# Optimization experiments

Hardware: AMD Instinct MI355X
Metric: run time of the kernel (lower is better)

## Reference

```python
import jax, jax.numpy as jnp
import numpy as np

B, T, E, S = 16, 2048, 1024, 2000
HID = 150
GI = 3 * E


def _mlp(x, W1, b1, W2, b2, W3, b3):
    # Score module: Linear->ReLU->(Dropout eval=id)->Linear->ReLU->(Dropout)->Linear(->1)
    h = jax.nn.relu(x @ W1 + b1)
    h = jax.nn.relu(h @ W2 + b2)
    return h @ W3 + b3


def setup_inputs() -> dict:
    key = jax.random.key(0)
    ks = jax.random.split(key, 16)
    batch_embeds = jax.random.normal(ks[0], (B, T, E), dtype=jnp.float32)
    starts = jnp.sort(jax.random.randint(ks[1], (B, S), 0, T - 33), axis=-1)
    lengths = jax.random.randint(ks[2], (B, S), 0, 24)
    num_spans = jax.random.randint(ks[3], (B,), 1, S + 1)
    sc = 0.02
    p = lambda k, shape: jax.random.normal(k, shape, dtype=jnp.float32) * sc
    return {
        "batch_embeds": batch_embeds,
        "starts": starts,
        "lengths": lengths,
        "num_spans": num_spans,
        "Wa1": p(ks[4], (E, HID)), "ba1": jnp.zeros((HID,), jnp.float32),
        "Wa2": p(ks[5], (HID, HID)), "ba2": jnp.zeros((HID,), jnp.float32),
        "Wa3": p(ks[6], (HID, 1)), "ba3": jnp.zeros((1,), jnp.float32),
        "Ws1": p(ks[7], (GI, HID)), "bs1": jnp.zeros((HID,), jnp.float32),
        "Ws2": p(ks[8], (HID, HID)), "bs2": jnp.zeros((HID,), jnp.float32),
        "Ws3": p(ks[9], (HID, 1)), "bs3": jnp.zeros((1,), jnp.float32),
    }


def reference(batch_embeds, starts, lengths, num_spans,
              Wa1, ba1, Wa2, ba2, Wa3, ba3,
              Ws1, bs1, Ws2, bs2, Ws3, bs3):
    # attention score per token: [B,T,1]
    attns = _mlp(batch_embeds, Wa1, ba1, Wa2, ba2, Wa3, ba3)
    weighted = batch_embeds * attns  # [B,T,E]
    # prefix sums turn the ragged per-span sum into two gathers per span
    csum = jnp.cumsum(weighted, axis=1)
    csum = jnp.concatenate([jnp.zeros_like(csum[:, :1]), csum], axis=1)  # [B,T+1,E]
    ends = starts + lengths  # inclusive end index, < T
    g_start = jnp.take_along_axis(batch_embeds, starts[..., None], axis=1)  # [B,S,E]
    g_end = jnp.take_along_axis(batch_embeds, ends[..., None], axis=1)      # [B,S,E]
    span_sum = (jnp.take_along_axis(csum, (ends + 1)[..., None], axis=1)
                - jnp.take_along_axis(csum, starts[..., None], axis=1))     # [B,S,E]
    span_emb = jnp.concatenate([g_start, g_end, span_sum], axis=-1)  # [B,S,3E]
    # zero-pad spans beyond each document's span count (matches torch zeros padding)
    mask = (jnp.arange(span_emb.shape[1])[None, :] < num_spans[:, None])[..., None]
    span_emb = jnp.where(mask, span_emb, jnp.zeros((), span_emb.dtype))
    mention_scores = _mlp(span_emb, Ws1, bs1, Ws2, bs2, Ws3, bs3)  # [B,S,1]
    return span_emb, mention_scores
```

## Files before the change

kernel.cpp:

```cpp
#include <hip/hip_runtime.h>
#include <hip/hip_bf16.h>

#define B_   16
#define T_   2048
#define E_   1024
#define S_   2000
#define HID_ 150
#define GI_  3072

typedef __attribute__((ext_vector_type(8))) short short8;
typedef __attribute__((ext_vector_type(4))) float f32x4;

constexpr int NPAD  = 160;
constexpr int LSTR  = 168;
constexpr int MROWS = 64;

__device__ __forceinline__ void gload16(const void* gsrc, void* ldst) {
    __builtin_amdgcn_global_load_lds(
        (const __attribute__((address_space(1))) unsigned int*)gsrc,
        (__attribute__((address_space(3))) unsigned int*)ldst,
        16, 0, 0);
}

__device__ __forceinline__ short8 pack8(float4 a, float4 b) {
    union { __hip_bfloat162 h[4]; short8 s; } u;
    u.h[0] = __float22bfloat162_rn(make_float2(a.x, a.y));
    u.h[1] = __float22bfloat162_rn(make_float2(a.z, a.w));
    u.h[2] = __float22bfloat162_rn(make_float2(b.x, b.y));
    u.h[3] = __float22bfloat162_rn(make_float2(b.z, b.w));
    return u.s;
}

__device__ __forceinline__ short8 pack8v(f32x4 a, f32x4 b) {
    union { __hip_bfloat162 h[4]; short8 s; } u;
    u.h[0] = __float22bfloat162_rn(make_float2(a.x, a.y));
    u.h[1] = __float22bfloat162_rn(make_float2(a.z, a.w));
    u.h[2] = __float22bfloat162_rn(make_float2(b.x, b.y));
    u.h[3] = __float22bfloat162_rn(make_float2(b.z, b.w));
    return u.s;
}

__device__ __forceinline__ void bf16x8_f32(short8 m, f32x4& lo, f32x4& hi) {
    union { short8 s; __hip_bfloat162 h[4]; } u; u.s = m;
    float2 f0 = __bfloat1622float2(u.h[0]);
    float2 f1 = __bfloat1622float2(u.h[1]);
    float2 f2 = __bfloat1622float2(u.h[2]);
    float2 f3 = __bfloat1622float2(u.h[3]);
    lo = (f32x4){f0.x, f0.y, f1.x, f1.y};
    hi = (f32x4){f2.x, f2.y, f3.x, f3.y};
}

__global__ __launch_bounds__(256)
void transpose_all(const float* __restrict__ Wa1, const float* __restrict__ Wa2,
                   const float* __restrict__ Ws1, const float* __restrict__ Ws2,
                   __hip_bfloat16* __restrict__ Wt1a, __hip_bfloat16* __restrict__ Wt2a,
                   __hip_bfloat16* __restrict__ Wt1s, __hip_bfloat16* __restrict__ Wt2s,
                   float* __restrict__ zerobuf)
{
    const int s0 = 160 * 1024, s1 = 160 * 160, s2 = 160 * 3072, s3 = 160 * 160;
    int i = blockIdx.x * 256 + threadIdx.x;
    if (i < s0) {
        int n = i >> 10, k = i & 1023;
        Wt1a[i] = __float2bfloat16(n < HID_ ? Wa1[k * HID_ + n] : 0.f);
    } else if (i < s0 + s1) {
        int j = i - s0, n = j / 160, k = j - n * 160;
        Wt2a[j] = __float2bfloat16((n < HID_ && k < HID_) ? Wa2[k * HID_ + n] : 0.f);
    } else if (i < s0 + s1 + s2) {
        int j = i - s0 - s1, n = j / 3072, k = j - n * 3072;
        Wt1s[j] = __float2bfloat16(n < HID_ ? Ws1[k * HID_ + n] : 0.f);
    } else if (i < s0 + s1 + s2 + s3) {
        int j = i - s0 - s1 - s2, n = j / 160, k = j - n * 160;
        Wt2s[j] = __float2bfloat16((n < HID_ && k < HID_) ? Ws2[k * HID_ + n] : 0.f);
    } else if (i < s0 + s1 + s2 + s3 + 1024) {
        zerobuf[i - s0 - s1 - s2 - s3] = 0.f;
    }
}

template<int K1>
__global__ __launch_bounds__(256, 2)
void mlp_mfma(const float* __restrict__ xin,
              const __hip_bfloat16* __restrict__ Wt1, const float* __restrict__ b1,
              const __hip_bfloat16* __restrict__ Wt2, const float* __restrict__ b2,
              const float* __restrict__ W3, const float* __restrict__ b3,
              float* __restrict__ outp)
{
    constexpr int NC  = K1 / 64;
    constexpr int ACH = 64 * 64 * 4;
    constexpr int BCH = 160 * 64 * 2;
    __shared__ __align__(16) char smem[2 * ACH + 2 * BCH];

    const int tid  = threadIdx.x;
    const int lane = tid & 63;
    const int w    = tid >> 6;
    const int rg   = w >> 1;
    const int cg   = w & 1;
    const int lr   = lane & 15;
    const int hi   = lane >> 4;

    const long long row0 = (long long)blockIdx.x * MROWS;

    auto stageA = [&](int bi, int c) {
        char* dst = smem + bi * ACH;
#pragma unroll
        for (int j = 0; j < 4; ++j) {
            const int row  = (w * 4 + j) * 4 + (lane >> 4);
            const int slot = (lane & 15) ^ (row & 7);
            gload16(xin + (row0 + row) * (long long)K1 + c * 64 + slot * 4,
                    dst + (w * 4 + j) * 1024);
        }
    };
    auto stageB = [&](int bi, int c) {
        char* dst = smem + 2 * ACH + bi * BCH;
#pragma unroll
        for (int j = 0; j < 5; ++j) {
            const int nrow = (w * 5 + j) * 8 + (lane >> 3);
            const int slot = (lane & 7) ^ (nrow & 7);
            gload16(Wt1 + (long long)nrow * K1 + c * 64 + slot * 8,
                    dst + (w * 5 + j) * 1024);
        }
    };

    f32x4 acc[2][5];
#pragma unroll
    for (int rt = 0; rt < 2; ++rt)
#pragma unroll
        for (int nt = 0; nt < 5; ++nt) acc[rt][nt] = (f32x4){0.f, 0.f, 0.f, 0.f};

    stageA(0, 0);
    stageB(0, 0);

    for (int c = 0; c < NC; ++c) {
        __syncthreads();
        if (c + 1 < NC) { stageA((c + 1) & 1, c + 1); stageB((c + 1) & 1, c + 1); }
        const int bi = c & 1;
        const char* sA = smem + bi * ACH;
        const char* sB = smem + 2 * ACH + bi * BCH;
#pragma unroll
        for (int ks = 0; ks < 2; ++ks) {
            short8 bfr[5];
#pragma unroll
            for (int nt = 0; nt < 5; ++nt) {
                const int nrow = cg * 80 + nt * 16 + lr;
                const int slot = (ks * 4 + hi) ^ (nrow & 7);
                bfr[nt] = *(const short8*)(sB + nrow * 128 + slot * 16);
            }
#pragma unroll
            for (int rt = 0; rt < 2; ++rt) {
                const int r = rg * 32 + rt * 16 + lr;
                const int s0i = (ks * 8 + hi * 2) ^ (r & 7);
                const int s1i = (ks * 8 + hi * 2 + 1) ^ (r & 7);
                float4 a0 = *(const float4*)(sA + r * 256 + s0i * 16);
                float4 a1 = *(const float4*)(sA + r * 256 + s1i * 16);
                short8 afr = pack8(a0, a1);
#pragma unroll
                for (int nt = 0; nt < 5; ++nt)
                    acc[rt][nt] = __builtin_amdgcn_mfma_f32_16x16x32_bf16(
                        afr, bfr[nt], acc[rt][nt], 0, 0, 0);
            }
        }
    }
    __syncthreads();

    __hip_bfloat16* hl = (__hip_bfloat16*)smem;

#pragma unroll
    for (int nt = 0; nt < 5; ++nt) {
        const int ch = cg * 80 + nt * 16 + lr;
        const float bb = (ch < HID_) ? b1[ch] : 0.f;
#pragma unroll
        for (int rt = 0; rt < 2; ++rt)
#pragma unroll
            for (int r4 = 0; r4 < 4; ++r4) {
                const int row = rg * 32 + rt * 16 + hi * 4 + r4;
                float h = acc[rt][nt][r4] + bb;
                hl[row * LSTR + ch] = __float2bfloat16(h > 0.f ? h : 0.f);
            }
    }
    __syncthreads();

    f32x4 acc2[2][5];
#pragma unroll
    for (int rt = 0; rt < 2; ++rt)
#pragma unroll
        for (int nt = 0; nt < 5; ++nt) acc2[rt][nt] = (f32x4){0.f, 0.f, 0.f, 0.f};

#pragma unroll
    for (int ks = 0; ks < 5; ++ks) {
        const int k0 = ks * 32 + hi * 8;
        short8 bfr[5];
#pragma unroll
        for (int nt = 0; nt < 5; ++nt)
            bfr[nt] = *(const short8*)(Wt2 + (cg * 80 + nt * 16 + lr) * NPAD + k0);
#pragma unroll
        for (int rt = 0; rt < 2; ++rt) {
            short8 afr = *(const short8*)&hl[(rg * 32 + rt * 16 + lr) * LSTR + k0];
#pragma unroll
            for (int nt = 0; nt < 5; ++nt)
                acc2[rt][nt] = __builtin_amdgcn_mfma_f32_16x16x32_bf16(
                    afr, bfr[nt], acc2[rt][nt], 0, 0, 0);
        }
    }
    __syncthreads();

#pragma unroll
    for (int nt = 0; nt < 5; ++nt) {
        const int ch = cg * 80 + nt * 16 + lr;
        const float bb = (ch < HID_) ? b2[ch] : 0.f;
#pragma unroll
        for (int rt = 0; rt < 2; ++rt)
#pragma unroll
            for (int r4 = 0; r4 < 4; ++r4) {
                const int row = rg * 32 + rt * 16 + hi * 4 + r4;
                float h = acc2[rt][nt][r4] + bb;
                hl[row * LSTR + ch] = __float2bfloat16(h > 0.f ? h : 0.f);
            }
    }
    __syncthreads();

    {
        const int row = tid >> 2, quad = tid & 3;
        const int kb = quad * 38;
        const int ke = (kb + 38 > HID_) ? HID_ : kb + 38;
        float s = 0.f;
        for (int k = kb; k < ke; ++k)
            s += __bfloat162float(hl[row * LSTR + k]) * W3[k];
        s += __shfl_xor(s, 1);
        s += __shfl_xor(s, 2);
        if (quad == 0) outp[row0 + row] = s + b3[0];
    }
}

__global__ __launch_bounds__(256)
void wsum_tiles(const float* __restrict__ x, const float* __restrict__ attn,
                float* __restrict__ P)
{
    const int b = blockIdx.x >> 5, tile = blockIdx.x & 31, q = threadIdx.x;
    const float* xb = x + ((long long)b * T_ + tile * 64) * E_ + q * 4;
    const float* ab = attn + b * T_ + tile * 64;
    f32x4 a0 = (f32x4){0.f, 0.f, 0.f, 0.f}, a1 = a0;
#pragma unroll 8
    for (int t = 0; t < 64; t += 2) {
        a0 += ab[t]     * *(const f32x4*)(xb + (long long)t * E_);
        a1 += ab[t + 1] * *(const f32x4*)(xb + (long long)(t + 1) * E_);
    }
    *(f32x4*)(P + ((long long)(b * 32 + tile)) * E_ + q * 4) = a0 + a1;
}

__global__ __launch_bounds__(256)
void wcumsum(const float* __restrict__ x, const float* __restrict__ attn,
             const float* __restrict__ P, __hip_bfloat16* __restrict__ csum)
{
    const int b = blockIdx.x >> 5, tile = blockIdx.x & 31, q = threadIdx.x;
    f32x4 pfx = (f32x4){0.f, 0.f, 0.f, 0.f};
    for (int tau = 0; tau < tile; ++tau)
        pfx += *(const f32x4*)(P + ((long long)(b * 32 + tau)) * E_ + q * 4);
    const float* xb = x + ((long long)b * T_ + tile * 64) * E_ + q * 4;
    __hip_bfloat16* cb = csum + ((long long)b * T_ + tile * 64) * E_ + q * 4;
    const float* ab = attn + b * T_ + tile * 64;
    f32x4 acc = pfx;
#pragma unroll 4
    for (int t = 0; t < 64; ++t) {
        acc += ab[t] * *(const f32x4*)(xb + (long long)t * E_);
        union { __hip_bfloat162 h[2]; uint2 u; } cv;
        cv.h[0] = __float22bfloat162_rn(make_float2(acc.x, acc.y));
        cv.h[1] = __float22bfloat162_rn(make_float2(acc.z, acc.w));
        *(uint2*)(cb + (long long)t * E_) = cv.u;
    }
}

__global__ __launch_bounds__(512, 4)
void span_score(const float* __restrict__ x, const __hip_bfloat16* __restrict__ csum,
                const float* __restrict__ zrow,
                const int* __restrict__ starts, const int* __restrict__ lengths,
                const int* __restrict__ nspans,
                const __hip_bfloat16* __restrict__ Wt1, const float* __restrict__ b1,
                const __hip_bfloat16* __restrict__ Wt2, const float* __restrict__ b2,
                const float* __restrict__ W3, const float* __restrict__ b3,
                float* __restrict__ spanout, float* __restrict__ scoreout)
{
    __shared__ __align__(16) char smem[58112];
    int* stL = (int*)(smem + 57344);
    int* enL = (int*)(smem + 57600);
    int* bL  = (int*)(smem + 57856);

    const int tid  = threadIdx.x;
    const int lane = tid & 63;
    const int w    = tid >> 6;
    const int rg   = w >> 1;
    const int cg   = w & 1;
    const int lr   = lane & 15;
    const int hi   = lane >> 4;

    int bid = blockIdx.x;
    {
        const int qq = 500 / 8, rr = 500 % 8;
        const int xcd = bid % 8, i = bid / 8;
        bid = (xcd < rr ? xcd * (qq + 1) : rr * (qq + 1) + (xcd - rr) * qq) + i;
    }
    const int span0 = bid * 64;

    if (tid < 64) {
        const int sp = span0 + tid;
        const int b  = sp / S_;
        const int s  = sp - b * S_;
        const bool val = s < nspans[b];
        const int st = val ? starts[sp] : 0;
        stL[tid] = st;
        enL[tid] = val ? (st + lengths[sp]) : -1;
        bL[tid]  = b;
    }
    __syncthreads();

    const int r    = tid >> 3;
    const int q    = tid & 7;
    const int st_r = stL[r];
    const int en_r = enL[r];
    const bool valid = en_r >= st_r;
    const long long sp_r = span0 + r;
    const float* xb = x + (long long)bL[r] * T_ * E_;
    const __hip_bfloat16* cbh = csum + (long long)bL[r] * T_ * E_;
    const __hip_bfloat16* zrh = (const __hip_bfloat16*)zrow;

    const float* px_st = valid ? xb + (long long)st_r * E_ : zrow;
    const float* px_en = valid ? xb + (long long)en_r * E_ : zrow;
    const __hip_bfloat16* pc_en = valid ? cbh + (long long)en_r * E_ : zrh;
    const __hip_bfloat16* pc_st = (valid && st_r > 0) ? cbh + (long long)(st_r - 1) * E_ : zrh;

    auto ldreg = [&](int c, f32x4& l0, f32x4& l1, short8& m0, short8& m1) {
        const int off = (c & 15) * 64 + q * 8;
        if (c < 32) {
            const float* s1 = (c < 16) ? px_st : px_en;
            l0 = *(const f32x4*)(s1 + off);
            l1 = *(const f32x4*)(s1 + off + 4);
        } else {
            m0 = *(const short8*)(pc_en + off);
            m1 = *(const short8*)(pc_st + off);
        }
    };
    auto emit = [&](int bi, int c, f32x4 l0, f32x4 l1, short8 m0, short8 m1) {
        f32x4 v0, v1;
        if (c < 32) { v0 = l0; v1 = l1; }
        else {
            f32x4 e0, e1, s0, s1v;
            bf16x8_f32(m0, e0, e1);
            bf16x8_f32(m1, s0, s1v);
            v0 = e0 - s0; v1 = e1 - s1v;
        }
        float* orow = spanout + sp_r * (3 * E_) + c * 64 + q * 8;
        *(f32x4*)orow       = v0;
        *(f32x4*)(orow + 4) = v1;
        *(short8*)(smem + bi * 8192 + r * 128 + ((q ^ (r & 7)) * 16)) = pack8v(v0, v1);
    };
    auto stageB = [&](int bi, int c) {
        char* dst = smem + 16384 + bi * 20480;
#pragma unroll
        for (int j = 0; j < 3; ++j) {
            const int idx = w * 3 + j;
            if (idx < 20) {
                const int nrow = idx * 8 + (lane >> 3);
                const int slot = (lane & 7) ^ (nrow & 7);
                gload16(Wt1 + (long long)nrow * GI_ + c * 64 + slot * 8,
                        dst + idx * 1024);
            }
        }
    };

    f32x4 acc[5];
#pragma unroll
    for (int nt = 0; nt < 5; ++nt) acc[nt] = (f32x4){0.f, 0.f, 0.f, 0.f};

    f32x4 pA0, pA1;  short8 mA0, mA1;
    f32x4 pB0, pB1;  short8 mB0, mB1;

    stageB(0, 0);
    asm volatile("" ::: "memory");
    ldreg(0, pA0, pA1, mA0, mA1);
    emit(0, 0, pA0, pA1, mA0, mA1);
    ldreg(1, pB0, pB1, mB0, mB1);

    auto mfma_block = [&](int bi) {
        const char* sAc = smem + bi * 8192;
        const char* sBc = smem + 16384 + bi * 20480;
#pragma unroll
        for (int ks = 0; ks < 2; ++ks) {
            short8 bfr[5];
#pragma unroll
            for (int nt = 0; nt < 5; ++nt) {
                const int nrow = cg * 80 + nt * 16 + lr;
                const int slot = (ks * 4 + hi) ^ (nrow & 7);
                bfr[nt] = *(const short8*)(sBc + nrow * 128 + slot * 16);
            }
            const int r2 = rg * 16 + lr;
            const int sl = (ks * 4 + hi) ^ (r2 & 7);
            short8 afr = *(const short8*)(sAc + r2 * 128 + sl * 16);
#pragma unroll
            for (int nt = 0; nt < 5; ++nt)
                acc[nt] = __builtin_amdgcn_mfma_f32_16x16x32_bf16(
                    afr, bfr[nt], acc[nt], 0, 0, 0);
        }
    };

    auto phase = [&](int c, f32x4& u0, f32x4& u1, short8& um0, short8& um1,
                     f32x4& f0, f32x4& f1, short8& fm0, short8& fm1) {
        asm volatile("s_waitcnt vmcnt(4) lgkmcnt(0)" ::: "memory");
        __builtin_amdgcn_s_barrier();
        const int bi = c & 1;
        if (c + 1 < 48) {
            stageB(bi ^ 1, c + 1);
            asm volatile("" ::: "memory");
            if (c + 2 < 48) ldreg(c + 2, f0, f1, fm0, fm1);
            asm volatile("" ::: "memory");
            emit(bi ^ 1, c + 1, u0, u1, um0, um1);
        }
        mfma_block(bi);
    };

    for (int cc = 0; cc < 46; cc += 2) {
        phase(cc,     pB0, pB1, mB0, mB1, pA0, pA1, mA0, mA1);
        phase(cc + 1, pA0, pA1, mA0, mA1, pB0, pB1, mB0, mB1);
    }
    phase(46, pB0, pB1, mB0, mB1, pA0, pA1, mA0, mA1);
    asm volatile("s_waitcnt vmcnt(2) lgkmcnt(0)" ::: "memory");
    __builtin_amdgcn_s_barrier();
    mfma_block(1);

    asm volatile("s_waitcnt lgkmcnt(0)" ::: "memory");
    __builtin_amdgcn_s_barrier();

    __hip_bfloat16* hl = (__hip_bfloat16*)smem;

#pragma unroll
    for (int nt = 0; nt < 5; ++nt) {
        const int ch = cg * 80 + nt * 16 + lr;
        const float bb = (ch < HID_) ? b1[ch] : 0.f;
#pragma unroll
        for (int r4 = 0; r4 < 4; ++r4) {
            const int row = rg * 16 + hi * 4 + r4;
            float h = acc[nt][r4] + bb;
            hl[row * LSTR + ch] = __float2bfloat16(h > 0.f ? h : 0.f);
        }
    }
    __syncthreads();

    f32x4 acc2[5];
#pragma unroll
    for (int nt = 0; nt < 5; ++nt) acc2[nt] = (f32x4){0.f, 0.f, 0.f, 0.f};

#pragma unroll
    for (int ks = 0; ks < 5; ++ks) {
        const int k0 = ks * 32 + hi * 8;
        short8 bfr[5];
#pragma unroll
        for (int nt = 0; nt < 5; ++nt)
            bfr[nt] = *(const short8*)(Wt2 + (cg * 80 + nt * 16 + lr) * NPAD + k0);
        short8 afr = *(const short8*)&hl[(rg * 16 + lr) * LSTR + k0];
#pragma unroll
        for (int nt = 0; nt < 5; ++nt)
            acc2[nt] = __builtin_amdgcn_mfma_f32_16x16x32_bf16(
                afr, bfr[nt], acc2[nt], 0, 0, 0);
    }
    __syncthreads();

#pragma unroll
    for (int nt = 0; nt < 5; ++nt) {
        const int ch = cg * 80 + nt * 16 + lr;
        const float bb = (ch < HID_) ? b2[ch] : 0.f;
#pragma unroll
        for (int r4 = 0; r4 < 4; ++r4) {
            const int row = rg * 16 + hi * 4 + r4;
            float h = acc2[nt][r4] + bb;
            hl[row * LSTR + ch] = __float2bfloat16(h > 0.f ? h : 0.f);
        }
    }
    __syncthreads();

    {
        const int row = tid >> 3, oct = tid & 7;
        const int kb = oct * 19;
        const int ke = (kb + 19 > HID_) ? HID_ : kb + 19;
        float s = 0.f;
        for (int k = kb; k < ke; ++k)
            s += __bfloat162float(hl[row * LSTR + k]) * W3[k];
        s += __shfl_xor(s, 1);
        s += __shfl_xor(s, 2);
        s += __shfl_xor(s, 4);
        if (oct == 0) scoreout[span0 + row] = s + b3[0];
    }
}

extern "C" void kernel_launch(void* const* d_in, const int* in_sizes, int n_in,
                              void* d_out, int out_size, void* d_ws, size_t ws_size,
                              hipStream_t stream) {
    const float* x       = (const float*)d_in[0];
    const int*   starts  = (const int*)d_in[1];
    const int*   lengths = (const int*)d_in[2];
    const int*   nspans  = (const int*)d_in[3];
    const float* Wa1 = (const float*)d_in[4];
    const float* ba1 = (const float*)d_in[5];
    const float* Wa2 = (const float*)d_in[6];
    const float* ba2 = (const float*)d_in[7];
    const float* Wa3 = (const float*)d_in[8];
    const float* ba3 = (const float*)d_in[9];
    const float* Ws1 = (const float*)d_in[10];
    const float* bs1 = (const float*)d_in[11];
    const float* Ws2 = (const float*)d_in[12];
    const float* bs2 = (const float*)d_in[13];
    const float* Ws3 = (const float*)d_in[14];
    const float* bs3 = (const float*)d_in[15];

    float* out        = (float*)d_out;
    float* out_scores = out + (long long)B_ * S_ * 3 * E_;

    char* ws = (char*)d_ws;
    float*          attn    = (float*)ws;
    __hip_bfloat16* Wt1a    = (__hip_bfloat16*)(ws + 131072);
    __hip_bfloat16* Wt2a    = (__hip_bfloat16*)(ws + 458752);
    __hip_bfloat16* Wt1s    = (__hip_bfloat16*)(ws + 509952);
    __hip_bfloat16* Wt2s    = (__hip_bfloat16*)(ws + 1492992);
    float*          zerobuf = (float*)(ws + 1544192);
    float*          Ptile   = (float*)(ws + 2097152);
    __hip_bfloat16* csum    = (__hip_bfloat16*)(ws + 4194304);

    transpose_all<<<2765, 256, 0, stream>>>(Wa1, Wa2, Ws1, Ws2,
                                            Wt1a, Wt2a, Wt1s, Wt2s, zerobuf);

    mlp_mfma<E_><<<(B_ * T_) / MROWS, 256, 0, stream>>>
        (x, Wt1a, ba1, Wt2a, ba2, Wa3, ba3, attn);

    wsum_tiles<<<B_ * 32, 256, 0, stream>>>(x, attn, Ptile);
    wcumsum   <<<B_ * 32, 256, 0, stream>>>(x, attn, Ptile, csum);

    span_score<<<500, 512, 0, stream>>>
        (x, csum, zerobuf, starts, lengths, nspans,
         Wt1s, bs1, Wt2s, bs2, Ws3, bs3, out, out_scores);
}
```

Baseline: 274.9 us.

## Fuse per-tile weighted sums into attention MLP kernel; nontemporal span stores

The attention-score MLP kernel now keeps its 64 per-row scores in shared memory and, after computing them, re-reads its own 64-row x tile to produce the per-tile weighted sum P directly. This removes the separate wsum_tiles launch and its extra pass over x, though x is still re-read from global memory (likely L2-resident). Separately, the fp32 span_emb output stores use nontemporal stores to reduce cache pollution on the large streaming write. The fused epilogue adds work and a barrier at the tail of each MLP block.

```diff
diff --git a/kernel.cpp b/kernel.cpp
--- a/kernel.cpp
+++ b/kernel.cpp
@@ -82,7 +82,7 @@
               const __hip_bfloat16* __restrict__ Wt1, const float* __restrict__ b1,
               const __hip_bfloat16* __restrict__ Wt2, const float* __restrict__ b2,
               const float* __restrict__ W3, const float* __restrict__ b3,
-              float* __restrict__ outp)
+              float* __restrict__ outp, float* __restrict__ Pout)
 {
     constexpr int NC  = K1 / 64;
     constexpr int ACH = 64 * 64 * 4;
@@ -162,6 +162,7 @@
     __syncthreads();
 
     __hip_bfloat16* hl = (__hip_bfloat16*)smem;
+    float* att_l = (float*)(smem + 24576);
 
 #pragma unroll
     for (int nt = 0; nt < 5; ++nt) {
@@ -226,24 +227,23 @@
             s += __bfloat162float(hl[row * LSTR + k]) * W3[k];
         s += __shfl_xor(s, 1);
         s += __shfl_xor(s, 2);
-        if (quad == 0) outp[row0 + row] = s + b3[0];
-    }
-}
-
-__global__ __launch_bounds__(256)
-void wsum_tiles(const float* __restrict__ x, const float* __restrict__ attn,
-                float* __restrict__ P)
-{
-    const int b = blockIdx.x >> 5, tile = blockIdx.x & 31, q = threadIdx.x;
-    const float* xb = x + ((long long)b * T_ + tile * 64) * E_ + q * 4;
-    const float* ab = attn + b * T_ + tile * 64;
-    f32x4 a0 = (f32x4){0.f, 0.f, 0.f, 0.f}, a1 = a0;
-#pragma unroll 8
-    for (int t = 0; t < 64; t += 2) {
-        a0 += ab[t]     * *(const f32x4*)(xb + (long long)t * E_);
-        a1 += ab[t + 1] * *(const f32x4*)(xb + (long long)(t + 1) * E_);
-    }
-    *(f32x4*)(P + ((long long)(b * 32 + tile)) * E_ + q * 4) = a0 + a1;
+        if (quad == 0) {
+            outp[row0 + row] = s + b3[0];
+            att_l[row] = s + b3[0];
+        }
+    }
+    __syncthreads();
+
+    {
+        const float* xb2 = xin + row0 * (long long)K1 + tid * 4;
+        f32x4 a0 = (f32x4){0.f, 0.f, 0.f, 0.f}, a1 = a0;
+#pragma unroll 4
+        for (int t = 0; t < 64; t += 2) {
+            a0 += att_l[t]     * *(const f32x4*)(xb2 + (long long)t * K1);
+            a1 += att_l[t + 1] * *(const f32x4*)(xb2 + (long long)(t + 1) * K1);
+        }
+        *(f32x4*)(Pout + (long long)blockIdx.x * K1 + tid * 4) = a0 + a1;
+    }
 }
 
 __global__ __launch_bounds__(256)
@@ -347,8 +347,8 @@
             v0 = e0 - s0; v1 = e1 - s1v;
         }
         float* orow = spanout + sp_r * (3 * E_) + c * 64 + q * 8;
-        *(f32x4*)orow       = v0;
-        *(f32x4*)(orow + 4) = v1;
+        __builtin_nontemporal_store(v0, (f32x4*)orow);
+        __builtin_nontemporal_store(v1, (f32x4*)(orow + 4));
         *(short8*)(smem + bi * 8192 + r * 128 + ((q ^ (r & 7)) * 16)) = pack8v(v0, v1);
     };
     auto stageB = [&](int bi, int c) {
@@ -525,10 +525,9 @@
                                             Wt1a, Wt2a, Wt1s, Wt2s, zerobuf);
 
     mlp_mfma<E_><<<(B_ * T_) / MROWS, 256, 0, stream>>>
-        (x, Wt1a, ba1, Wt2a, ba2, Wa3, ba3, attn);
-
-    wsum_tiles<<<B_ * 32, 256, 0, stream>>>(x, attn, Ptile);
-    wcumsum   <<<B_ * 32, 256, 0, stream>>>(x, attn, Ptile, csum);
+        (x, Wt1a, ba1, Wt2a, ba2, Wa3, ba3, attn, Ptile);
+
+    wcumsum<<<B_ * 32, 256, 0, stream>>>(x, attn, Ptile, csum);
 
     span_score<<<500, 512, 0, stream>>>
         (x, csum, zerobuf, starts, lengths, nspans,
```

Result: faster. 255.2 us (-7.2%).
